# Performance work log

Hardware: AMD Instinct MI355X
Metric: run time of the kernel (lower is better)

Reference implementation:

```python
import jax, jax.numpy as jnp
import numpy as np

B, S, HID = 2, 2048, 1024
NH = 16
HD = HID // NH  # 64


def rope_cos_sin(seq_len, dim, dtype=jnp.float32):
    inv_freq = 1.0 / (10000.0 ** (jnp.arange(0, dim, 2, dtype=jnp.float32) / dim))
    t = jnp.arange(seq_len, dtype=jnp.float32)
    freqs = jnp.outer(t, inv_freq)            # [S, dim/2]
    emb = jnp.concatenate([freqs, freqs], -1)  # [S, dim]
    return jnp.cos(emb).astype(dtype), jnp.sin(emb).astype(dtype)


def rotate_half(x):
    x1, x2 = jnp.split(x, 2, axis=-1)
    return jnp.concatenate([-x2, x1], axis=-1)


def apply_rope(x, cos, sin):
    # x: [B, H, S, D]; cos/sin: [S, D]
    return x * cos[None, None] + rotate_half(x) * sin[None, None]


def setup_inputs() -> dict:
    key = jax.random.key(0)
    ks = jax.random.split(key, 7)
    scale = 0.02
    return {
        "hidden_states": jax.random.normal(ks[0], (B, S, HID), jnp.float32),
        "attention_mask": jnp.zeros((B, 1, 1, S), jnp.float32),
        "Wq": jax.random.normal(ks[1], (HID, HID), jnp.float32) * scale,
        "bq": jnp.zeros((HID,), jnp.float32),
        "Wk": jax.random.normal(ks[2], (HID, HID), jnp.float32) * scale,
        "bk": jnp.zeros((HID,), jnp.float32),
        "Wv": jax.random.normal(ks[3], (HID, HID), jnp.float32) * scale,
        "bv": jnp.zeros((HID,), jnp.float32),
    }


def reference(hidden_states, attention_mask, Wq, bq, Wk, bk, Wv, bv):
    def split_heads(x):  # [B,S,HID] -> [B,H,S,D]
        return x.reshape(B, S, NH, HD).transpose(0, 2, 1, 3)

    q = split_heads(hidden_states @ Wq + bq)
    k = split_heads(hidden_states @ Wk + bk)
    v = split_heads(hidden_states @ Wv + bv)

    q = q * (HD ** -0.5)
    cos, sin = rope_cos_sin(S, HD, q.dtype)
    q = apply_rope(q, cos, sin)
    k = apply_rope(k, cos, sin)

    scores = jnp.einsum("bhqd,bhkd->bhqk", q, k) + attention_mask
    probs = jax.nn.softmax(scores, axis=-1)
    ctx = jnp.einsum("bhqk,bhkd->bhqd", probs, v)
    ctx = ctx.transpose(0, 2, 1, 3).reshape(B, S, HID)
    return ctx
```

## Files before the change

### kernel.cpp

```cpp
#include <hip/hip_runtime.h>
#include <math.h>

namespace {
constexpr int B_ = 2, S_ = 2048, HID_ = 1024, NH_ = 16, HD_ = 64;
constexpr int M_ = B_ * S_;
constexpr int QSZ = B_ * NH_ * S_ * HD_;
constexpr int TBL = S_ * (HD_ / 2);
constexpr float LOG2E = 1.4426950408889634f;

typedef float f32x4 __attribute__((ext_vector_type(4)));
typedef __bf16 bf16x8 __attribute__((ext_vector_type(8)));
typedef unsigned int u32x4 __attribute__((ext_vector_type(4)));
typedef unsigned short u16;

__device__ inline u16 f2bf(float x) {
  unsigned int u = __float_as_uint(x);
  return (u16)((u + 0x7fffu + ((u >> 16) & 1u)) >> 16);
}
__device__ inline float bf2f(u16 h) {
  return __uint_as_float(((unsigned int)h) << 16);
}

typedef __attribute__((address_space(1))) const unsigned int as1_u32;
typedef __attribute__((address_space(3))) unsigned int as3_u32;
__device__ __forceinline__ void gll16(const void* g, void* l) {
  __builtin_amdgcn_global_load_lds((as1_u32*)g, (as3_u32*)l, 16, 0, 0);
}

__device__ __forceinline__ void swap32(unsigned int& a, unsigned int& b) {
  asm("v_permlane32_swap_b32 %0, %1" : "+v"(a), "+v"(b));
}
__device__ __forceinline__ void swap16(unsigned int& a, unsigned int& b) {
  asm("v_permlane16_swap_b32 %0, %1" : "+v"(a), "+v"(b));
}
__device__ __forceinline__ unsigned int cvtpk(float lo, float hi) {
  unsigned int r;
  asm("v_cvt_pk_bf16_f32 %0, %1, %2" : "=v"(r) : "v"(lo), "v"(hi));
  return r;
}

__global__ __launch_bounds__(256)
void prep_kernel(const float* __restrict__ hs, u16* __restrict__ hh,
                 const float* __restrict__ Wq, const float* __restrict__ Wk,
                 const float* __restrict__ Wv, u16* __restrict__ wt,
                 float* __restrict__ ct, float* __restrict__ st) {
  __shared__ float tile[64][65];
  const int bid = blockIdx.x;
  const int t = threadIdx.x;
  if (bid < 4096) {
    size_t e = (size_t)bid * 256 + t;
    float4 v = *(const float4*)&hs[e * 4];
    short4 hi = {(short)f2bf(v.x), (short)f2bf(v.y), (short)f2bf(v.z), (short)f2bf(v.w)};
    *(short4*)&hh[e * 4] = hi;
  } else if (bid < 4864) {
    int r = bid - 4096;
    int bx = r & 15, by = (r >> 4) & 15, bz = r >> 8;
    const float* W = bz == 0 ? Wq : bz == 1 ? Wk : Wv;
    int k0 = bx * 64, n0 = by * 64;
    int lrow = t >> 4, lcol = (t & 15) * 4;
#pragma unroll
    for (int i = 0; i < 4; ++i) {
      float4 v = *(const float4*)&W[(size_t)(k0 + lrow + i * 16) * HID_ + n0 + lcol];
      tile[lrow + i * 16][lcol + 0] = v.x;
      tile[lrow + i * 16][lcol + 1] = v.y;
      tile[lrow + i * 16][lcol + 2] = v.z;
      tile[lrow + i * 16][lcol + 3] = v.w;
    }
    __syncthreads();
    int n = t >> 2, ks = (t & 3) * 16;
    u16 tmp[16];
#pragma unroll
    for (int j = 0; j < 16; ++j) tmp[j] = f2bf(tile[ks + j][n]);
    u16* dst = &wt[((size_t)bz * 1024 + n0 + n) * 1024 + k0 + ks];
    ((uint4*)dst)[0] = ((uint4*)tmp)[0];
    ((uint4*)dst)[1] = ((uint4*)tmp)[1];
  } else {
    int e = (bid - 4864) * 256 + t;
    int s = e >> 5, i = e & 31;
    float inv = 1.0f / powf(10000.0f, (float)(2 * i) / (float)HD_);
    float ang = (float)s * inv;
    double a = (double)ang;
    ct[e] = (float)cos(a);
    st[e] = (float)sin(a);
  }
}

__global__ __launch_bounds__(256)
void proj_gemm_kernel(const u16* __restrict__ Ah, const u16* __restrict__ Wt,
                      const float* __restrict__ bq, const float* __restrict__ bk,
                      const float* __restrict__ bv,
                      const float* __restrict__ ct, const float* __restrict__ st,
                      u16* __restrict__ qw, u16* __restrict__ kw, u16* __restrict__ vt) {
  __shared__ u16 sAh[2][128 * 64];
  __shared__ u16 sB[2][128 * 64];
  const int tid = threadIdx.x;
  const int wave = tid >> 6, lane = tid & 63;
  const int lr = lane & 15, lg = lane >> 4;

  int bid = blockIdx.x;
  int swz = (bid & 7) * 96 + (bid >> 3);
  const int gx = swz / 24, gy = swz % 24;
  const int m0 = gx * 128;
  const int ng0 = gy * 128;

  size_t aoff[4], boff[4];
  int c16[4];
#pragma unroll
  for (int i = 0; i < 4; ++i) {
    int c = i * 256 + tid;
    int row = c >> 3, ks = c & 7;
    int kph = (ks ^ (row & 7)) * 8;
    aoff[i] = (size_t)(m0 + row) * HID_ + kph;
    boff[i] = (size_t)(ng0 + row) * HID_ + kph;
    c16[i] = c * 16;
  }

  const int wr = (wave >> 1) * 64, wc = (wave & 1) * 64;
  int offA[4][2], offB[4][2];
#pragma unroll
  for (int f = 0; f < 4; ++f) {
    int ra = wr + f * 16 + lr;
    int rb = wc + f * 16 + lr;
#pragma unroll
    for (int kk = 0; kk < 2; ++kk) {
      offA[f][kk] = ra * 128 + (((kk * 4 + lg)) ^ (ra & 7)) * 16;
      offB[f][kk] = rb * 128 + (((kk * 4 + lg)) ^ (rb & 7)) * 16;
    }
  }

  f32x4 acc[4][4];
#pragma unroll
  for (int mf = 0; mf < 4; ++mf)
#pragma unroll
    for (int nf = 0; nf < 4; ++nf) acc[mf][nf] = (f32x4){0.f, 0.f, 0.f, 0.f};

#pragma unroll
  for (int i = 0; i < 4; ++i) {
    gll16(Ah + aoff[i], (char*)sAh[0] + c16[i]);
    gll16(Wt + boff[i], (char*)sB[0] + c16[i]);
  }
  __syncthreads();

  for (int t = 0; t < 16; ++t) {
    if (t < 15) {
      const int nb = (t + 1) & 1;
      const int k0n = (t + 1) * 64;
#pragma unroll
      for (int i = 0; i < 4; ++i) {
        gll16(Ah + aoff[i] + k0n, (char*)sAh[nb] + c16[i]);
        gll16(Wt + boff[i] + k0n, (char*)sB[nb] + c16[i]);
      }
      asm volatile("s_waitcnt vmcnt(8)" ::: "memory");
    } else {
      asm volatile("s_waitcnt vmcnt(0)" ::: "memory");
    }
    __builtin_amdgcn_s_barrier();
    __builtin_amdgcn_sched_barrier(0);

    const char* sa = (const char*)sAh[t & 1];
    const char* sb = (const char*)sB[t & 1];
#pragma unroll
    for (int kk = 0; kk < 2; ++kk) {
      bf16x8 a_h[4], bb[4];
#pragma unroll
      for (int f = 0; f < 4; ++f) {
        a_h[f] = *(const bf16x8*)(sa + offA[f][kk]);
        bb[f] = *(const bf16x8*)(sb + offB[f][kk]);
      }
      __builtin_amdgcn_s_setprio(1);
#pragma unroll
      for (int mf = 0; mf < 4; ++mf)
#pragma unroll
        for (int nf = 0; nf < 4; ++nf)
          acc[mf][nf] = __builtin_amdgcn_mfma_f32_16x16x32_bf16(a_h[mf], bb[nf], acc[mf][nf], 0, 0, 0);
      __builtin_amdgcn_s_setprio(0);
    }
    __builtin_amdgcn_sched_barrier(0);
    __builtin_amdgcn_s_barrier();
  }

  const int which = gy >> 3;
  const int colm = (gy & 7) * 128 + wc;
  const int h = colm >> 6;
  const float* bias = which == 0 ? bq : which == 1 ? bk : bv;
  const float scale = which == 0 ? 0.125f * LOG2E : 1.0f;

  if (which < 2) {
    u16* oh = which == 0 ? qw : kw;
#pragma unroll
    for (int mf = 0; mf < 4; ++mf) {
#pragma unroll
      for (int r = 0; r < 4; ++r) {
        int m = m0 + wr + mf * 16 + lg * 4 + r;
        int b = m >> 11, s = m & (S_ - 1);
        size_t rowb = (((size_t)b * NH_ + h) * S_ + s) * HD_;
#pragma unroll
        for (int nf = 0; nf < 2; ++nf) {
          int d = nf * 16 + lr;
          float x1 = acc[mf][nf][r] + bias[colm + d];
          float x2 = acc[mf][nf + 2][r] + bias[colm + d + 32];
          float cth = ct[s * 32 + d], sth = st[s * 32 + d];
          oh[rowb + d]      = f2bf((x1 * cth - x2 * sth) * scale);
          oh[rowb + d + 32] = f2bf((x2 * cth + x1 * sth) * scale);
        }
      }
    }
  } else {
#pragma unroll
    for (int mf = 0; mf < 4; ++mf) {
      int mB = m0 + wr + mf * 16 + lg * 4;
      int b = mB >> 11, s0 = mB & (S_ - 1);
#pragma unroll
      for (int nf = 0; nf < 4; ++nf) {
        int d = nf * 16 + lr;
        float bi = bias[colm + d];
        ushort4 pk;
        pk.x = f2bf(acc[mf][nf][0] + bi);
        pk.y = f2bf(acc[mf][nf][1] + bi);
        pk.z = f2bf(acc[mf][nf][2] + bi);
        pk.w = f2bf(acc[mf][nf][3] + bi);
        *(ushort4*)&vt[(((size_t)b * NH_ + h) * HD_ + d) * S_ + s0] = pk;
      }
    }
  }
}

__global__ __launch_bounds__(256, 2)
void attn_mfma_kernel(const u16* __restrict__ qw, const u16* __restrict__ kw,
                      const u16* __restrict__ vt, const float* __restrict__ mask,
                      float* __restrict__ outp) {
  __shared__ __align__(16) char smem[40960];
  constexpr int MS = 32768;
  const int tid = threadIdx.x;
  const int wave = tid >> 6, lane = tid & 63;
  const int lr = lane & 15, lg = lane >> 4;

  const int bid = blockIdx.x;
  const int idx = bid >> 3;
  const int bh = (bid & 7) * 4 + (idx >> 4);
  const int q0 = (idx & 15) * 128;
  const int b = bh >> 4, h = bh & 15;
  const size_t hb = (size_t)bh * S_ * HD_;

  {
    const float* mrow = mask + (size_t)b * S_ + tid * 8;
    float4 v0 = *(const float4*)mrow;
    float4 v1 = *(const float4*)(mrow + 4);
    v0.x *= LOG2E; v0.y *= LOG2E; v0.z *= LOG2E; v0.w *= LOG2E;
    v1.x *= LOG2E; v1.y *= LOG2E; v1.z *= LOG2E; v1.w *= LOG2E;
    *(float4*)(smem + MS + tid * 32) = v0;
    *(float4*)(smem + MS + tid * 32 + 16) = v1;
  }

  bf16x8 aq[2][2];
#pragma unroll
  for (int qb = 0; qb < 2; ++qb) {
    size_t base = hb + (size_t)(q0 + wave * 32 + qb * 16 + lr) * HD_ + lg * 8;
    aq[qb][0] = *(const bf16x8*)&qw[base];
    aq[qb][1] = *(const bf16x8*)&qw[base + 32];
  }

  bf16x8 ones_f;
  {
    unsigned int w = (lr == 0) ? 0x3F803F80u : 0u;
    u32x4 f = {w, w, w, w};
    ones_f = *(bf16x8*)&f;
  }

  f32x4 O[2][4], O4[2];
  float mrun[2];
#pragma unroll
  for (int qb = 0; qb < 2; ++qb) {
    mrun[qb] = -INFINITY;
    O4[qb] = (f32x4){0.f, 0.f, 0.f, 0.f};
#pragma unroll
    for (int dt = 0; dt < 4; ++dt) O[qb][dt] = (f32x4){0.f, 0.f, 0.f, 0.f};
  }

  size_t kgo[2], vgo[2];
  int klo_[2], vlo_[2];
#pragma unroll
  for (int i = 0; i < 2; ++i) {
    int a = i * 4096 + tid * 16;
    int row = a >> 7, seg = (a >> 4) & 7;
    int sseg = (seg ^ (row & 7)) * 8;
    kgo[i] = (size_t)row * HD_ + sseg;
    klo_[i] = a;
    vgo[i] = (size_t)row * S_ + sseg;
    vlo_[i] = 8192 + a;
  }

  const int sw = (lr & 7) << 4;

#define STAGE_KV(T, BASE)                                                   \
  {                                                                         \
    _Pragma("unroll") for (int i = 0; i < 2; ++i) {                         \
      gll16(kw + hb + kgo[i] + (size_t)(T) * 64 * HD_, smem + (BASE) + klo_[i]); \
      gll16(vt + hb + vgo[i] + (T) * 64, smem + (BASE) + vlo_[i]);          \
    }                                                                       \
  }

  STAGE_KV(0, 0);
  __syncthreads();

  for (int t = 0; t < 32; ++t) {
    const int base = (t & 1) << 14;
    if (t < 31) {
      STAGE_KV(t + 1, ((t + 1) & 1) << 14);
      asm volatile("s_waitcnt vmcnt(4)" ::: "memory");
    } else {
      asm volatile("s_waitcnt vmcnt(0)" ::: "memory");
    }
    __builtin_amdgcn_s_barrier();
    __builtin_amdgcn_sched_barrier(0);

    f32x4 sc[2][4];
#pragma unroll
    for (int qb = 0; qb < 2; ++qb)
#pragma unroll
      for (int c = 0; c < 4; ++c) sc[qb][c] = (f32x4){0.f, 0.f, 0.f, 0.f};
    __builtin_amdgcn_s_setprio(1);
#pragma unroll
    for (int t2 = 0; t2 < 2; ++t2) {
#pragma unroll
      for (int c = 0; c < 4; ++c) {
        int off = base + ((c * 16 + lr) << 7) + ((t2 * 64 + lg * 16) ^ sw);
        bf16x8 kf = *(const bf16x8*)(smem + off);
        sc[0][c] = __builtin_amdgcn_mfma_f32_16x16x32_bf16(kf, aq[0][t2], sc[0][c], 0, 0, 0);
        sc[1][c] = __builtin_amdgcn_mfma_f32_16x16x32_bf16(kf, aq[1][t2], sc[1][c], 0, 0, 0);
      }
    }
    __builtin_amdgcn_s_setprio(0);

    f32x4 mk[4];
#pragma unroll
    for (int c = 0; c < 4; ++c)
      mk[c] = *(const f32x4*)(smem + MS + (t * 64 + c * 16 + lg * 4) * 4);

    bf16x8 pf[2][2];
#pragma unroll
    for (int qb = 0; qb < 2; ++qb) {
      float mx = -INFINITY;
#pragma unroll
      for (int c = 0; c < 4; ++c) {
        sc[qb][c] += mk[c];
#pragma unroll
        for (int r = 0; r < 4; ++r) mx = fmaxf(mx, sc[qb][c][r]);
      }
      mx = fmaxf(mx, __shfl_xor(mx, 16));
      mx = fmaxf(mx, __shfl_xor(mx, 32));
      if (mx > mrun[qb] + 8.f) {
        float corr = __builtin_amdgcn_exp2f(mrun[qb] - mx);
        mrun[qb] = mx;
        O4[qb] *= corr;
#pragma unroll
        for (int dt = 0; dt < 4; ++dt) O[qb][dt] *= corr;
      }
#pragma unroll
      for (int c = 0; c < 4; ++c)
#pragma unroll
        for (int r = 0; r < 4; ++r)
          sc[qb][c][r] = __builtin_amdgcn_exp2f(sc[qb][c][r] - mrun[qb]);

#pragma unroll
      for (int kt = 0; kt < 2; ++kt) {
        unsigned int x0 = cvtpk(sc[qb][2 * kt][0], sc[qb][2 * kt][1]);
        unsigned int x1 = cvtpk(sc[qb][2 * kt + 1][0], sc[qb][2 * kt + 1][1]);
        unsigned int y0 = cvtpk(sc[qb][2 * kt][2], sc[qb][2 * kt][3]);
        unsigned int y1 = cvtpk(sc[qb][2 * kt + 1][2], sc[qb][2 * kt + 1][3]);
        swap32(x0, x1);
        swap16(x0, x1);
        swap32(y0, y1);
        swap16(y0, y1);
        u32x4 f = {x0, y0, x1, y1};
        pf[qb][kt] = *(bf16x8*)&f;
      }
    }

    __builtin_amdgcn_s_setprio(1);
#pragma unroll
    for (int kt = 0; kt < 2; ++kt) {
      O4[0] = __builtin_amdgcn_mfma_f32_16x16x32_bf16(ones_f, pf[0][kt], O4[0], 0, 0, 0);
      O4[1] = __builtin_amdgcn_mfma_f32_16x16x32_bf16(ones_f, pf[1][kt], O4[1], 0, 0, 0);
#pragma unroll
      for (int dt = 0; dt < 4; ++dt) {
        int off = base + 8192 + ((dt * 16 + lr) << 7) + ((kt * 64 + lg * 16) ^ sw);
        bf16x8 vf = *(const bf16x8*)(smem + off);
        O[0][dt] = __builtin_amdgcn_mfma_f32_16x16x32_bf16(vf, pf[0][kt], O[0][dt], 0, 0, 0);
        O[1][dt] = __builtin_amdgcn_mfma_f32_16x16x32_bf16(vf, pf[1][kt], O[1][dt], 0, 0, 0);
      }
    }
    __builtin_amdgcn_s_setprio(0);

    __builtin_amdgcn_sched_barrier(0);
    __builtin_amdgcn_s_barrier();
  }

#pragma unroll
  for (int qb = 0; qb < 2; ++qb) {
    float l = __shfl(O4[qb][0], lr, 64);
    float inv = 1.0f / l;
    int s = q0 + wave * 32 + qb * 16 + lr;
    size_t rowb = ((size_t)b * S_ + s) * HID_ + h * HD_;
#pragma unroll
    for (int dt = 0; dt < 4; ++dt) {
      float4 r;
      r.x = O[qb][dt][0] * inv;
      r.y = O[qb][dt][1] * inv;
      r.z = O[qb][dt][2] * inv;
      r.w = O[qb][dt][3] * inv;
      *(float4*)&outp[rowb + dt * 16 + lg * 4] = r;
    }
  }
#undef STAGE_KV
}

}

extern "C" void kernel_launch(void* const* d_in, const int* in_sizes, int n_in,
                              void* d_out, int out_size, void* d_ws, size_t ws_size,
                              hipStream_t stream) {
  const float* hs   = (const float*)d_in[0];
  const float* mask = (const float*)d_in[1];
  const float* Wq   = (const float*)d_in[2];
  const float* bq   = (const float*)d_in[3];
  const float* Wk   = (const float*)d_in[4];
  const float* bk   = (const float*)d_in[5];
  const float* Wv   = (const float*)d_in[6];
  const float* bv   = (const float*)d_in[7];

  u16* qw = (u16*)d_ws;
  u16* kw = qw + QSZ;
  u16* vt = kw + QSZ;
  u16* hh = vt + QSZ;
  u16* wt = hh + (size_t)M_ * HID_;
  float* ct = (float*)(wt + (size_t)3 * 1024 * 1024);
  float* st = ct + TBL;

  prep_kernel<<<5120, 256, 0, stream>>>(hs, hh, Wq, Wk, Wv, wt, ct, st);

  proj_gemm_kernel<<<768, 256, 0, stream>>>(hh, wt, bq, bk, bv, ct, st, qw, kw, vt);

  attn_mfma_kernel<<<512, 256, 0, stream>>>(qw, kw, vt, mask, (float*)d_out);
}
```

Baseline: 106.8 us.

## Halve attention query tile and drop K/V double buffering for more occupancy

Each attention block now processes 64 queries (16 per wave) instead of 128, doubling the grid and halving per-wave accumulators and score registers. The K/V double-buffered async staging with vmcnt waits is replaced by a single LDS buffer loaded between two __syncthreads each iteration, cutting LDS use. This aims to raise occupancy and let more resident waves hide latency, at the cost of losing explicit load/compute overlap and doubling K/V reloads per query.

```diff
diff --git a/kernel.cpp b/kernel.cpp
--- a/kernel.cpp
+++ b/kernel.cpp
@@ -225,20 +225,20 @@
   }
 }
 
-__global__ __launch_bounds__(256, 2)
+__global__ __launch_bounds__(256)
 void attn_mfma_kernel(const u16* __restrict__ qw, const u16* __restrict__ kw,
                       const u16* __restrict__ vt, const float* __restrict__ mask,
                       float* __restrict__ outp) {
-  __shared__ __align__(16) char smem[40960];
-  constexpr int MS = 32768;
+  __shared__ __align__(16) char smem[24576];
+  constexpr int VTB = 8192, MS = 16384;
   const int tid = threadIdx.x;
   const int wave = tid >> 6, lane = tid & 63;
   const int lr = lane & 15, lg = lane >> 4;
 
   const int bid = blockIdx.x;
   const int idx = bid >> 3;
-  const int bh = (bid & 7) * 4 + (idx >> 4);
-  const int q0 = (idx & 15) * 128;
+  const int bh = (bid & 7) * 4 + (idx >> 5);
+  const int q0 = (idx & 31) * 64;
   const int b = bh >> 4, h = bh & 15;
   const size_t hb = (size_t)bh * S_ * HD_;
 
@@ -252,12 +252,11 @@
     *(float4*)(smem + MS + tid * 32 + 16) = v1;
   }
 
-  bf16x8 aq[2][2];
-#pragma unroll
-  for (int qb = 0; qb < 2; ++qb) {
-    size_t base = hb + (size_t)(q0 + wave * 32 + qb * 16 + lr) * HD_ + lg * 8;
-    aq[qb][0] = *(const bf16x8*)&qw[base];
-    aq[qb][1] = *(const bf16x8*)&qw[base + 32];
+  bf16x8 aq[2];
+  {
+    size_t base = hb + (size_t)(q0 + wave * 16 + lr) * HD_ + lg * 8;
+    aq[0] = *(const bf16x8*)&qw[base];
+    aq[1] = *(const bf16x8*)&qw[base + 32];
   }
 
   bf16x8 ones_f;
@@ -267,15 +266,11 @@
     ones_f = *(bf16x8*)&f;
   }
 
-  f32x4 O[2][4], O4[2];
-  float mrun[2];
-#pragma unroll
-  for (int qb = 0; qb < 2; ++qb) {
-    mrun[qb] = -INFINITY;
-    O4[qb] = (f32x4){0.f, 0.f, 0.f, 0.f};
-#pragma unroll
-    for (int dt = 0; dt < 4; ++dt) O[qb][dt] = (f32x4){0.f, 0.f, 0.f, 0.f};
-  }
+  f32x4 O[4], O4;
+  float mrun = -INFINITY;
+  O4 = (f32x4){0.f, 0.f, 0.f, 0.f};
+#pragma unroll
+  for (int dt = 0; dt < 4; ++dt) O[dt] = (f32x4){0.f, 0.f, 0.f, 0.f};
 
   size_t kgo[2], vgo[2];
   int klo_[2], vlo_[2];
@@ -287,47 +282,31 @@
     kgo[i] = (size_t)row * HD_ + sseg;
     klo_[i] = a;
     vgo[i] = (size_t)row * S_ + sseg;
-    vlo_[i] = 8192 + a;
+    vlo_[i] = VTB + a;
   }
 
   const int sw = (lr & 7) << 4;
 
-#define STAGE_KV(T, BASE)                                                   \
-  {                                                                         \
-    _Pragma("unroll") for (int i = 0; i < 2; ++i) {                         \
-      gll16(kw + hb + kgo[i] + (size_t)(T) * 64 * HD_, smem + (BASE) + klo_[i]); \
-      gll16(vt + hb + vgo[i] + (T) * 64, smem + (BASE) + vlo_[i]);          \
-    }                                                                       \
-  }
-
-  STAGE_KV(0, 0);
-  __syncthreads();
-
   for (int t = 0; t < 32; ++t) {
-    const int base = (t & 1) << 14;
-    if (t < 31) {
-      STAGE_KV(t + 1, ((t + 1) & 1) << 14);
-      asm volatile("s_waitcnt vmcnt(4)" ::: "memory");
-    } else {
-      asm volatile("s_waitcnt vmcnt(0)" ::: "memory");
-    }
-    __builtin_amdgcn_s_barrier();
-    __builtin_amdgcn_sched_barrier(0);
-
-    f32x4 sc[2][4];
-#pragma unroll
-    for (int qb = 0; qb < 2; ++qb)
-#pragma unroll
-      for (int c = 0; c < 4; ++c) sc[qb][c] = (f32x4){0.f, 0.f, 0.f, 0.f};
+    __syncthreads();
+#pragma unroll
+    for (int i = 0; i < 2; ++i) {
+      gll16(kw + hb + kgo[i] + (size_t)t * 64 * HD_, smem + klo_[i]);
+      gll16(vt + hb + vgo[i] + t * 64, smem + vlo_[i]);
+    }
+    __syncthreads();
+
+    f32x4 sc[4];
+#pragma unroll
+    for (int c = 0; c < 4; ++c) sc[c] = (f32x4){0.f, 0.f, 0.f, 0.f};
     __builtin_amdgcn_s_setprio(1);
 #pragma unroll
     for (int t2 = 0; t2 < 2; ++t2) {
 #pragma unroll
       for (int c = 0; c < 4; ++c) {
-        int off = base + ((c * 16 + lr) << 7) + ((t2 * 64 + lg * 16) ^ sw);
+        int off = ((c * 16 + lr) << 7) + ((t2 * 64 + lg * 16) ^ sw);
         bf16x8 kf = *(const bf16x8*)(smem + off);
-        sc[0][c] = __builtin_amdgcn_mfma_f32_16x16x32_bf16(kf, aq[0][t2], sc[0][c], 0, 0, 0);
-        sc[1][c] = __builtin_amdgcn_mfma_f32_16x16x32_bf16(kf, aq[1][t2], sc[1][c], 0, 0, 0);
+        sc[c] = __builtin_amdgcn_mfma_f32_16x16x32_bf16(kf, aq[t2], sc[c], 0, 0, 0);
       }
     }
     __builtin_amdgcn_s_setprio(0);
@@ -337,82 +316,72 @@
     for (int c = 0; c < 4; ++c)
       mk[c] = *(const f32x4*)(smem + MS + (t * 64 + c * 16 + lg * 4) * 4);
 
-    bf16x8 pf[2][2];
-#pragma unroll
-    for (int qb = 0; qb < 2; ++qb) {
-      float mx = -INFINITY;
-#pragma unroll
-      for (int c = 0; c < 4; ++c) {
-        sc[qb][c] += mk[c];
-#pragma unroll
-        for (int r = 0; r < 4; ++r) mx = fmaxf(mx, sc[qb][c][r]);
-      }
-      mx = fmaxf(mx, __shfl_xor(mx, 16));
-      mx = fmaxf(mx, __shfl_xor(mx, 32));
-      if (mx > mrun[qb] + 8.f) {
-        float corr = __builtin_amdgcn_exp2f(mrun[qb] - mx);
-        mrun[qb] = mx;
-        O4[qb] *= corr;
-#pragma unroll
-        for (int dt = 0; dt < 4; ++dt) O[qb][dt] *= corr;
-      }
-#pragma unroll
-      for (int c = 0; c < 4; ++c)
-#pragma unroll
-        for (int r = 0; r < 4; ++r)
-          sc[qb][c][r] = __builtin_amdgcn_exp2f(sc[qb][c][r] - mrun[qb]);
-
-#pragma unroll
-      for (int kt = 0; kt < 2; ++kt) {
-        unsigned int x0 = cvtpk(sc[qb][2 * kt][0], sc[qb][2 * kt][1]);
-        unsigned int x1 = cvtpk(sc[qb][2 * kt + 1][0], sc[qb][2 * kt + 1][1]);
-        unsigned int y0 = cvtpk(sc[qb][2 * kt][2], sc[qb][2 * kt][3]);
-        unsigned int y1 = cvtpk(sc[qb][2 * kt + 1][2], sc[qb][2 * kt + 1][3]);
-        swap32(x0, x1);
-        swap16(x0, x1);
-        swap32(y0, y1);
-        swap16(y0, y1);
-        u32x4 f = {x0, y0, x1, y1};
-        pf[qb][kt] = *(bf16x8*)&f;
-      }
+    float mx = -INFINITY;
+#pragma unroll
+    for (int c = 0; c < 4; ++c) {
+      sc[c] += mk[c];
+#pragma unroll
+      for (int r = 0; r < 4; ++r) mx = fmaxf(mx, sc[c][r]);
+    }
+    mx = fmaxf(mx, __shfl_xor(mx, 16));
+    mx = fmaxf(mx, __shfl_xor(mx, 32));
+    if (mx > mrun + 8.f) {
+      float corr = __builtin_amdgcn_exp2f(mrun - mx);
+      mrun = mx;
+      O4 *= corr;
+#pragma unroll
+      for (int dt = 0; dt < 4; ++dt) O[dt] *= corr;
+    }
+#pragma unroll
+    for (int c = 0; c < 4; ++c)
+#pragma unroll
+      for (int r = 0; r < 4; ++r)
+        sc[c][r] = __builtin_amdgcn_exp2f(sc[c][r] - mrun);
+
+    bf16x8 pf[2];
+#pragma unroll
+    for (int kt = 0; kt < 2; ++kt) {
+      unsigned int x0 = cvtpk(sc[2 * kt][0], sc[2 * kt][1]);
+      unsigned int x1 = cvtpk(sc[2 * kt + 1][0], sc[2 * kt + 1][1]);
+      unsigned int y0 = cvtpk(sc[2 * kt][2], sc[2 * kt][3]);
+      unsigned int y1 = cvtpk(sc[2 * kt + 1][2], sc[2 * kt + 1][3]);
+      swap32(x0, x1);
+      swap16(x0, x1);
+      swap32(y0, y1);
+      swap16(y0, y1);
+      u32x4 f = {x0, y0, x1, y1};
+      pf[kt] = *(bf16x8*)&f;
     }
 
     __builtin_amdgcn_s_setprio(1);
 #pragma unroll
     for (int kt = 0; kt < 2; ++kt) {
-      O4[0] = __builtin_amdgcn_mfma_f32_16x16x32_bf16(ones_f, pf[0][kt], O4[0], 0, 0, 0);
-      O4[1] = __builtin_amdgcn_mfma_f32_16x16x32_bf16(ones_f, pf[1][kt], O4[1], 0, 0, 0);
+      O4 = __builtin_amdgcn_mfma_f32_16x16x32_bf16(ones_f, pf[kt], O4, 0, 0, 0);
 #pragma unroll
       for (int dt = 0; dt < 4; ++dt) {
-        int off = base + 8192 + ((dt * 16 + lr) << 7) + ((kt * 64 + lg * 16) ^ sw);
+        int off = VTB + ((dt * 16 + lr) << 7) + ((kt * 64 + lg * 16) ^ sw);
         bf16x8 vf = *(const bf16x8*)(smem + off);
-        O[0][dt] = __builtin_amdgcn_mfma_f32_16x16x32_bf16(vf, pf[0][kt], O[0][dt], 0, 0, 0);
-        O[1][dt] = __builtin_amdgcn_mfma_f32_16x16x32_bf16(vf, pf[1][kt], O[1][dt], 0, 0, 0);
+        O[dt] = __builtin_amdgcn_mfma_f32_16x16x32_bf16(vf, pf[kt], O[dt], 0, 0, 0);
       }
     }
     __builtin_amdgcn_s_setprio(0);
-
-    __builtin_amdgcn_sched_barrier(0);
-    __builtin_amdgcn_s_barrier();
-  }
-
-#pragma unroll
-  for (int qb = 0; qb < 2; ++qb) {
-    float l = __shfl(O4[qb][0], lr, 64);
+  }
+
+  {
+    float l = __shfl(O4[0], lr, 64);
     float inv = 1.0f / l;
-    int s = q0 + wave * 32 + qb * 16 + lr;
+    int s = q0 + wave * 16 + lr;
     size_t rowb = ((size_t)b * S_ + s) * HID_ + h * HD_;
 #pragma unroll
     for (int dt = 0; dt < 4; ++dt) {
       float4 r;
-      r.x = O[qb][dt][0] * inv;
-      r.y = O[qb][dt][1] * inv;
-      r.z = O[qb][dt][2] * inv;
-      r.w = O[qb][dt][3] * inv;
+      r.x = O[dt][0] * inv;
+      r.y = O[dt][1] * inv;
+      r.z = O[dt][2] * inv;
+      r.w = O[dt][3] * inv;
       *(float4*)&outp[rowb + dt * 16 + lg * 4] = r;
     }
   }
-#undef STAGE_KV
 }
 
 }
@@ -441,5 +410,5 @@
 
   proj_gemm_kernel<<<768, 256, 0, stream>>>(hh, wt, bq, bk, bv, ct, st, qw, kw, vt);
 
-  attn_mfma_kernel<<<512, 256, 0, stream>>>(qw, kw, vt, mask, (float*)d_out);
-}
+  attn_mfma_kernel<<<1024, 256, 0, stream>>>(qw, kw, vt, mask, (float*)d_out);
+}
```

Measured after the change: 114.7 us. +7.5%, slower.

## Split attention over two key halves and merge partials in a combine kernel

Applied to the files above, without the earlier changes.

Replaces the single attention kernel with a split-K (flash-decoding style) scheme: each block handles half the keys for a query tile, writing bf16 partial outputs plus a log-sum-exp. A second kernel merges the two halves into the final fp32 output. The key tile grows to 128 and the double-buffered async pipeline is replaced by single-buffer loads with two syncthreads per step. This doubles the grid to improve occupancy across CUs, at the cost of extra global traffic, a second launch, bf16 rounding of partials, and loss of load/compute overlap.

```diff
diff --git a/kernel.cpp b/kernel.cpp
--- a/kernel.cpp
+++ b/kernel.cpp
@@ -6,6 +6,7 @@
 constexpr int M_ = B_ * S_;
 constexpr int QSZ = B_ * NH_ * S_ * HD_;
 constexpr int TBL = S_ * (HD_ / 2);
+constexpr int NQI = B_ * NH_ * S_;
 constexpr float LOG2E = 1.4426950408889634f;
 
 typedef float f32x4 __attribute__((ext_vector_type(4)));
@@ -225,31 +226,29 @@
   }
 }
 
-__global__ __launch_bounds__(256, 2)
-void attn_mfma_kernel(const u16* __restrict__ qw, const u16* __restrict__ kw,
+__global__ __launch_bounds__(256)
+void attn_part_kernel(const u16* __restrict__ qw, const u16* __restrict__ kw,
                       const u16* __restrict__ vt, const float* __restrict__ mask,
-                      float* __restrict__ outp) {
-  __shared__ __align__(16) char smem[40960];
-  constexpr int MS = 32768;
+                      u16* __restrict__ part, float* __restrict__ Lb) {
+  __shared__ __align__(16) char smem[36864];
+  constexpr int VTB = 16384, MS = 32768;
   const int tid = threadIdx.x;
   const int wave = tid >> 6, lane = tid & 63;
   const int lr = lane & 15, lg = lane >> 4;
 
   const int bid = blockIdx.x;
   const int idx = bid >> 3;
-  const int bh = (bid & 7) * 4 + (idx >> 4);
-  const int q0 = (idx & 15) * 128;
-  const int b = bh >> 4, h = bh & 15;
+  const int bh = (bid & 7) * 4 + (idx >> 5);
+  const int q0 = ((idx >> 1) & 15) * 128;
+  const int sh = idx & 1;
+  const int kbase = sh * 1024;
+  const int b = bh >> 4;
   const size_t hb = (size_t)bh * S_ * HD_;
 
   {
-    const float* mrow = mask + (size_t)b * S_ + tid * 8;
-    float4 v0 = *(const float4*)mrow;
-    float4 v1 = *(const float4*)(mrow + 4);
+    float4 v0 = *(const float4*)(mask + (size_t)b * S_ + kbase + tid * 4);
     v0.x *= LOG2E; v0.y *= LOG2E; v0.z *= LOG2E; v0.w *= LOG2E;
-    v1.x *= LOG2E; v1.y *= LOG2E; v1.z *= LOG2E; v1.w *= LOG2E;
-    *(float4*)(smem + MS + tid * 32) = v0;
-    *(float4*)(smem + MS + tid * 32 + 16) = v1;
+    *(float4*)(smem + MS + tid * 16) = v0;
   }
 
   bf16x8 aq[2][2];
@@ -277,54 +276,47 @@
     for (int dt = 0; dt < 4; ++dt) O[qb][dt] = (f32x4){0.f, 0.f, 0.f, 0.f};
   }
 
-  size_t kgo[2], vgo[2];
-  int klo_[2], vlo_[2];
-#pragma unroll
-  for (int i = 0; i < 2; ++i) {
+  size_t kgo[4], vgo[4];
+  int klo_[4], vlo_[4];
+#pragma unroll
+  for (int i = 0; i < 4; ++i) {
     int a = i * 4096 + tid * 16;
-    int row = a >> 7, seg = (a >> 4) & 7;
-    int sseg = (seg ^ (row & 7)) * 8;
-    kgo[i] = (size_t)row * HD_ + sseg;
-    klo_[i] = a;
-    vgo[i] = (size_t)row * S_ + sseg;
-    vlo_[i] = 8192 + a;
+    {
+      int row = a >> 7, seg = (a >> 4) & 7;
+      kgo[i] = (size_t)row * HD_ + ((seg ^ (row & 7)) * 8);
+      klo_[i] = a;
+    }
+    {
+      int row = a >> 8, seg = (a >> 4) & 15;
+      int sg = (seg & 8) | ((seg & 7) ^ (row & 7));
+      vgo[i] = (size_t)row * S_ + sg * 8;
+      vlo_[i] = VTB + a;
+    }
   }
 
   const int sw = (lr & 7) << 4;
 
-#define STAGE_KV(T, BASE)                                                   \
-  {                                                                         \
-    _Pragma("unroll") for (int i = 0; i < 2; ++i) {                         \
-      gll16(kw + hb + kgo[i] + (size_t)(T) * 64 * HD_, smem + (BASE) + klo_[i]); \
-      gll16(vt + hb + vgo[i] + (T) * 64, smem + (BASE) + vlo_[i]);          \
-    }                                                                       \
-  }
-
-  STAGE_KV(0, 0);
-  __syncthreads();
-
-  for (int t = 0; t < 32; ++t) {
-    const int base = (t & 1) << 14;
-    if (t < 31) {
-      STAGE_KV(t + 1, ((t + 1) & 1) << 14);
-      asm volatile("s_waitcnt vmcnt(4)" ::: "memory");
-    } else {
-      asm volatile("s_waitcnt vmcnt(0)" ::: "memory");
-    }
-    __builtin_amdgcn_s_barrier();
-    __builtin_amdgcn_sched_barrier(0);
-
-    f32x4 sc[2][4];
+  for (int t = 0; t < 8; ++t) {
+    const int k0 = kbase + t * 128;
+    __syncthreads();
+#pragma unroll
+    for (int i = 0; i < 4; ++i) {
+      gll16(kw + hb + kgo[i] + (size_t)k0 * HD_, smem + klo_[i]);
+      gll16(vt + hb + vgo[i] + k0, smem + vlo_[i]);
+    }
+    __syncthreads();
+
+    f32x4 sc[2][8];
 #pragma unroll
     for (int qb = 0; qb < 2; ++qb)
 #pragma unroll
-      for (int c = 0; c < 4; ++c) sc[qb][c] = (f32x4){0.f, 0.f, 0.f, 0.f};
+      for (int c = 0; c < 8; ++c) sc[qb][c] = (f32x4){0.f, 0.f, 0.f, 0.f};
     __builtin_amdgcn_s_setprio(1);
 #pragma unroll
     for (int t2 = 0; t2 < 2; ++t2) {
 #pragma unroll
-      for (int c = 0; c < 4; ++c) {
-        int off = base + ((c * 16 + lr) << 7) + ((t2 * 64 + lg * 16) ^ sw);
+      for (int c = 0; c < 8; ++c) {
+        int off = ((c * 16 + lr) << 7) + ((t2 * 64 + lg * 16) ^ sw);
         bf16x8 kf = *(const bf16x8*)(smem + off);
         sc[0][c] = __builtin_amdgcn_mfma_f32_16x16x32_bf16(kf, aq[0][t2], sc[0][c], 0, 0, 0);
         sc[1][c] = __builtin_amdgcn_mfma_f32_16x16x32_bf16(kf, aq[1][t2], sc[1][c], 0, 0, 0);
@@ -332,17 +324,17 @@
     }
     __builtin_amdgcn_s_setprio(0);
 
-    f32x4 mk[4];
-#pragma unroll
-    for (int c = 0; c < 4; ++c)
-      mk[c] = *(const f32x4*)(smem + MS + (t * 64 + c * 16 + lg * 4) * 4);
-
-    bf16x8 pf[2][2];
+    f32x4 mk[8];
+#pragma unroll
+    for (int c = 0; c < 8; ++c)
+      mk[c] = *(const f32x4*)(smem + MS + (t * 128 + c * 16 + lg * 4) * 4);
+
+    bf16x8 pf[2][4];
 #pragma unroll
     for (int qb = 0; qb < 2; ++qb) {
       float mx = -INFINITY;
 #pragma unroll
-      for (int c = 0; c < 4; ++c) {
+      for (int c = 0; c < 8; ++c) {
         sc[qb][c] += mk[c];
 #pragma unroll
         for (int r = 0; r < 4; ++r) mx = fmaxf(mx, sc[qb][c][r]);
@@ -357,13 +349,13 @@
         for (int dt = 0; dt < 4; ++dt) O[qb][dt] *= corr;
       }
 #pragma unroll
-      for (int c = 0; c < 4; ++c)
+      for (int c = 0; c < 8; ++c)
 #pragma unroll
         for (int r = 0; r < 4; ++r)
           sc[qb][c][r] = __builtin_amdgcn_exp2f(sc[qb][c][r] - mrun[qb]);
 
 #pragma unroll
-      for (int kt = 0; kt < 2; ++kt) {
+      for (int kt = 0; kt < 4; ++kt) {
         unsigned int x0 = cvtpk(sc[qb][2 * kt][0], sc[qb][2 * kt][1]);
         unsigned int x1 = cvtpk(sc[qb][2 * kt + 1][0], sc[qb][2 * kt + 1][1]);
         unsigned int y0 = cvtpk(sc[qb][2 * kt][2], sc[qb][2 * kt][3]);
@@ -379,40 +371,74 @@
 
     __builtin_amdgcn_s_setprio(1);
 #pragma unroll
-    for (int kt = 0; kt < 2; ++kt) {
+    for (int kt = 0; kt < 4; ++kt) {
       O4[0] = __builtin_amdgcn_mfma_f32_16x16x32_bf16(ones_f, pf[0][kt], O4[0], 0, 0, 0);
       O4[1] = __builtin_amdgcn_mfma_f32_16x16x32_bf16(ones_f, pf[1][kt], O4[1], 0, 0, 0);
 #pragma unroll
       for (int dt = 0; dt < 4; ++dt) {
-        int off = base + 8192 + ((dt * 16 + lr) << 7) + ((kt * 64 + lg * 16) ^ sw);
+        int off = VTB + ((dt * 16 + lr) << 8) + ((kt * 64 + lg * 16) ^ sw);
         bf16x8 vf = *(const bf16x8*)(smem + off);
         O[0][dt] = __builtin_amdgcn_mfma_f32_16x16x32_bf16(vf, pf[0][kt], O[0][dt], 0, 0, 0);
         O[1][dt] = __builtin_amdgcn_mfma_f32_16x16x32_bf16(vf, pf[1][kt], O[1][dt], 0, 0, 0);
       }
     }
     __builtin_amdgcn_s_setprio(0);
-
-    __builtin_amdgcn_sched_barrier(0);
-    __builtin_amdgcn_s_barrier();
   }
 
 #pragma unroll
   for (int qb = 0; qb < 2; ++qb) {
     float l = __shfl(O4[qb][0], lr, 64);
     float inv = 1.0f / l;
+    float Lk = mrun[qb] + __log2f(l);
     int s = q0 + wave * 32 + qb * 16 + lr;
-    size_t rowb = ((size_t)b * S_ + s) * HID_ + h * HD_;
+    size_t qi = ((size_t)sh * 32 + bh) * S_ + s;
+    u16* pp = part + qi * HD_;
 #pragma unroll
     for (int dt = 0; dt < 4; ++dt) {
-      float4 r;
-      r.x = O[qb][dt][0] * inv;
-      r.y = O[qb][dt][1] * inv;
-      r.z = O[qb][dt][2] * inv;
-      r.w = O[qb][dt][3] * inv;
-      *(float4*)&outp[rowb + dt * 16 + lg * 4] = r;
-    }
-  }
-#undef STAGE_KV
+      ushort4 pk;
+      pk.x = f2bf(O[qb][dt][0] * inv);
+      pk.y = f2bf(O[qb][dt][1] * inv);
+      pk.z = f2bf(O[qb][dt][2] * inv);
+      pk.w = f2bf(O[qb][dt][3] * inv);
+      *(ushort4*)&pp[dt * 16 + lg * 4] = pk;
+    }
+    if (lg == 0) Lb[qi] = Lk;
+  }
+}
+
+__global__ __launch_bounds__(256)
+void attn_combine_kernel(const u16* __restrict__ part, const float* __restrict__ Lb,
+                         float* __restrict__ outp) {
+  int gid = blockIdx.x * 256 + threadIdx.x;
+  int qi = gid >> 3;
+  int dseg = (gid & 7) * 8;
+  int bh = qi >> 11, s = qi & (S_ - 1);
+  int b = bh >> 4, h = bh & 15;
+  float L0 = Lb[qi], L1 = Lb[NQI + qi];
+  float M = fmaxf(L0, L1);
+  float w0 = __builtin_amdgcn_exp2f(L0 - M);
+  float w1 = __builtin_amdgcn_exp2f(L1 - M);
+  float inv = 1.0f / (w0 + w1);
+  w0 *= inv;
+  w1 *= inv;
+  const u16* p0 = part + (size_t)qi * HD_ + dseg;
+  const u16* p1 = part + ((size_t)NQI + qi) * HD_ + dseg;
+  uint4 a0 = *(const uint4*)p0;
+  uint4 a1 = *(const uint4*)p1;
+  const u16* e0 = (const u16*)&a0;
+  const u16* e1 = (const u16*)&a1;
+  float4 r0, r1;
+  r0.x = bf2f(e0[0]) * w0 + bf2f(e1[0]) * w1;
+  r0.y = bf2f(e0[1]) * w0 + bf2f(e1[1]) * w1;
+  r0.z = bf2f(e0[2]) * w0 + bf2f(e1[2]) * w1;
+  r0.w = bf2f(e0[3]) * w0 + bf2f(e1[3]) * w1;
+  r1.x = bf2f(e0[4]) * w0 + bf2f(e1[4]) * w1;
+  r1.y = bf2f(e0[5]) * w0 + bf2f(e1[5]) * w1;
+  r1.z = bf2f(e0[6]) * w0 + bf2f(e1[6]) * w1;
+  r1.w = bf2f(e0[7]) * w0 + bf2f(e1[7]) * w1;
+  size_t ob = ((size_t)b * S_ + s) * HID_ + h * HD_ + dseg;
+  *(float4*)&outp[ob] = r0;
+  *(float4*)&outp[ob + 4] = r1;
 }
 
 }
@@ -436,10 +462,14 @@
   u16* wt = hh + (size_t)M_ * HID_;
   float* ct = (float*)(wt + (size_t)3 * 1024 * 1024);
   float* st = ct + TBL;
+  u16* part = (u16*)(st + TBL);
+  float* Lb = (float*)(part + (size_t)2 * NQI * HD_);
 
   prep_kernel<<<5120, 256, 0, stream>>>(hs, hh, Wq, Wk, Wv, wt, ct, st);
 
   proj_gemm_kernel<<<768, 256, 0, stream>>>(hh, wt, bq, bk, bv, ct, st, qw, kw, vt);
 
-  attn_mfma_kernel<<<512, 256, 0, stream>>>(qw, kw, vt, mask, (float*)d_out);
-}
+  attn_part_kernel<<<1024, 256, 0, stream>>>(qw, kw, vt, mask, part, Lb);
+
+  attn_combine_kernel<<<2048, 256, 0, stream>>>(part, Lb, (float*)d_out);
+}
```

Measured after the change: 146.1 us. 36.8% more time.

## Replace double-buffered 64-key pipeline with single-buffered 128-key tiles

Applied to the files above, without the earlier changes.

The attention kernel drops the double-buffered K/V prefetch that loaded 64-key tiles and instead loads 128-key tiles into one shared buffer, with a sync before and after each load. This halves the number of loop iterations and online-softmax rescale checks per block and gives the MFMA sequences more work between barriers. In exchange, global loads no longer overlap compute within a block, so latency hiding now depends on the other resident block. Register pressure also rises because the score and probability arrays double in size.

```diff
diff --git a/kernel.cpp b/kernel.cpp
--- a/kernel.cpp
+++ b/kernel.cpp
@@ -230,7 +230,7 @@
                       const u16* __restrict__ vt, const float* __restrict__ mask,
                       float* __restrict__ outp) {
   __shared__ __align__(16) char smem[40960];
-  constexpr int MS = 32768;
+  constexpr int VTB = 16384, MS = 32768;
   const int tid = threadIdx.x;
   const int wave = tid >> 6, lane = tid & 63;
   const int lr = lane & 15, lg = lane >> 4;
@@ -277,54 +277,46 @@
     for (int dt = 0; dt < 4; ++dt) O[qb][dt] = (f32x4){0.f, 0.f, 0.f, 0.f};
   }
 
-  size_t kgo[2], vgo[2];
-  int klo_[2], vlo_[2];
-#pragma unroll
-  for (int i = 0; i < 2; ++i) {
+  size_t kgo[4], vgo[4];
+  int klo_[4], vlo_[4];
+#pragma unroll
+  for (int i = 0; i < 4; ++i) {
     int a = i * 4096 + tid * 16;
-    int row = a >> 7, seg = (a >> 4) & 7;
-    int sseg = (seg ^ (row & 7)) * 8;
-    kgo[i] = (size_t)row * HD_ + sseg;
-    klo_[i] = a;
-    vgo[i] = (size_t)row * S_ + sseg;
-    vlo_[i] = 8192 + a;
+    {
+      int row = a >> 7, seg = (a >> 4) & 7;
+      kgo[i] = (size_t)row * HD_ + ((seg ^ (row & 7)) * 8);
+      klo_[i] = a;
+    }
+    {
+      int row = a >> 8, seg = (a >> 4) & 15;
+      int sg = (seg & 8) | ((seg & 7) ^ (row & 7));
+      vgo[i] = (size_t)row * S_ + sg * 8;
+      vlo_[i] = VTB + a;
+    }
   }
 
   const int sw = (lr & 7) << 4;
 
-#define STAGE_KV(T, BASE)                                                   \
-  {                                                                         \
-    _Pragma("unroll") for (int i = 0; i < 2; ++i) {                         \
-      gll16(kw + hb + kgo[i] + (size_t)(T) * 64 * HD_, smem + (BASE) + klo_[i]); \
-      gll16(vt + hb + vgo[i] + (T) * 64, smem + (BASE) + vlo_[i]);          \
-    }                                                                       \
-  }
-
-  STAGE_KV(0, 0);
-  __syncthreads();
-
-  for (int t = 0; t < 32; ++t) {
-    const int base = (t & 1) << 14;
-    if (t < 31) {
-      STAGE_KV(t + 1, ((t + 1) & 1) << 14);
-      asm volatile("s_waitcnt vmcnt(4)" ::: "memory");
-    } else {
-      asm volatile("s_waitcnt vmcnt(0)" ::: "memory");
-    }
-    __builtin_amdgcn_s_barrier();
-    __builtin_amdgcn_sched_barrier(0);
-
-    f32x4 sc[2][4];
+  for (int k0 = 0; k0 < S_; k0 += 128) {
+    __syncthreads();
+#pragma unroll
+    for (int i = 0; i < 4; ++i) {
+      gll16(kw + hb + kgo[i] + (size_t)k0 * HD_, smem + klo_[i]);
+      gll16(vt + hb + vgo[i] + k0, smem + vlo_[i]);
+    }
+    __syncthreads();
+
+    f32x4 sc[2][8];
 #pragma unroll
     for (int qb = 0; qb < 2; ++qb)
 #pragma unroll
-      for (int c = 0; c < 4; ++c) sc[qb][c] = (f32x4){0.f, 0.f, 0.f, 0.f};
+      for (int c = 0; c < 8; ++c) sc[qb][c] = (f32x4){0.f, 0.f, 0.f, 0.f};
     __builtin_amdgcn_s_setprio(1);
 #pragma unroll
     for (int t2 = 0; t2 < 2; ++t2) {
 #pragma unroll
-      for (int c = 0; c < 4; ++c) {
-        int off = base + ((c * 16 + lr) << 7) + ((t2 * 64 + lg * 16) ^ sw);
+      for (int c = 0; c < 8; ++c) {
+        int off = ((c * 16 + lr) << 7) + ((t2 * 64 + lg * 16) ^ sw);
         bf16x8 kf = *(const bf16x8*)(smem + off);
         sc[0][c] = __builtin_amdgcn_mfma_f32_16x16x32_bf16(kf, aq[0][t2], sc[0][c], 0, 0, 0);
         sc[1][c] = __builtin_amdgcn_mfma_f32_16x16x32_bf16(kf, aq[1][t2], sc[1][c], 0, 0, 0);
@@ -332,17 +324,17 @@
     }
     __builtin_amdgcn_s_setprio(0);
 
-    f32x4 mk[4];
-#pragma unroll
-    for (int c = 0; c < 4; ++c)
-      mk[c] = *(const f32x4*)(smem + MS + (t * 64 + c * 16 + lg * 4) * 4);
-
-    bf16x8 pf[2][2];
+    f32x4 mk[8];
+#pragma unroll
+    for (int c = 0; c < 8; ++c)
+      mk[c] = *(const f32x4*)(smem + MS + (k0 + c * 16 + lg * 4) * 4);
+
+    bf16x8 pf[2][4];
 #pragma unroll
     for (int qb = 0; qb < 2; ++qb) {
       float mx = -INFINITY;
 #pragma unroll
-      for (int c = 0; c < 4; ++c) {
+      for (int c = 0; c < 8; ++c) {
         sc[qb][c] += mk[c];
 #pragma unroll
         for (int r = 0; r < 4; ++r) mx = fmaxf(mx, sc[qb][c][r]);
@@ -357,13 +349,13 @@
         for (int dt = 0; dt < 4; ++dt) O[qb][dt] *= corr;
       }
 #pragma unroll
-      for (int c = 0; c < 4; ++c)
+      for (int c = 0; c < 8; ++c)
 #pragma unroll
         for (int r = 0; r < 4; ++r)
           sc[qb][c][r] = __builtin_amdgcn_exp2f(sc[qb][c][r] - mrun[qb]);
 
 #pragma unroll
-      for (int kt = 0; kt < 2; ++kt) {
+      for (int kt = 0; kt < 4; ++kt) {
         unsigned int x0 = cvtpk(sc[qb][2 * kt][0], sc[qb][2 * kt][1]);
         unsigned int x1 = cvtpk(sc[qb][2 * kt + 1][0], sc[qb][2 * kt + 1][1]);
         unsigned int y0 = cvtpk(sc[qb][2 * kt][2], sc[qb][2 * kt][3]);
@@ -379,21 +371,18 @@
 
     __builtin_amdgcn_s_setprio(1);
 #pragma unroll
-    for (int kt = 0; kt < 2; ++kt) {
+    for (int kt = 0; kt < 4; ++kt) {
       O4[0] = __builtin_amdgcn_mfma_f32_16x16x32_bf16(ones_f, pf[0][kt], O4[0], 0, 0, 0);
       O4[1] = __builtin_amdgcn_mfma_f32_16x16x32_bf16(ones_f, pf[1][kt], O4[1], 0, 0, 0);
 #pragma unroll
       for (int dt = 0; dt < 4; ++dt) {
-        int off = base + 8192 + ((dt * 16 + lr) << 7) + ((kt * 64 + lg * 16) ^ sw);
+        int off = VTB + ((dt * 16 + lr) << 8) + ((kt * 64 + lg * 16) ^ sw);
         bf16x8 vf = *(const bf16x8*)(smem + off);
         O[0][dt] = __builtin_amdgcn_mfma_f32_16x16x32_bf16(vf, pf[0][kt], O[0][dt], 0, 0, 0);
         O[1][dt] = __builtin_amdgcn_mfma_f32_16x16x32_bf16(vf, pf[1][kt], O[1][dt], 0, 0, 0);
       }
     }
     __builtin_amdgcn_s_setprio(0);
-
-    __builtin_amdgcn_sched_barrier(0);
-    __builtin_amdgcn_s_barrier();
   }
 
 #pragma unroll
@@ -412,7 +401,6 @@
       *(float4*)&outp[rowb + dt * 16 + lg * 4] = r;
     }
   }
-#undef STAGE_KV
 }
 
 }
```

New measurement: 105.8 us. No clear change (-0.9%).
